# Optimization experiments

Measured on AMD Instinct MI355X. Metric: run time of the kernel, lower is better.

The kernel has to match this reference:

```python
import jax, jax.numpy as jnp
import numpy as np

N_NODES = 100000
NEG_SLOPE = 0.2  # PyG GATConv default LeakyReLU slope


def gat_conv(x, src, dst, W, a_src, a_dst, bias, n):
    # x: [N, Fin] -> h: [N, Fout]; heads=1, concat=True (PyG defaults), add_self_loops=False
    h = x @ W
    alpha_s = h @ a_src  # [N]
    alpha_d = h @ a_dst  # [N]
    e = jax.nn.leaky_relu(alpha_s[src] + alpha_d[dst], NEG_SLOPE)  # [E]
    # segment-softmax over edges grouped by destination node
    m = jax.ops.segment_max(e, dst, num_segments=n)  # [N], -inf for isolated nodes (never gathered)
    ex = jnp.exp(e - m[dst])
    denom = jax.ops.segment_sum(ex, dst, num_segments=n)
    alpha = ex / denom[dst]  # [E]
    out = jax.ops.segment_sum(alpha[:, None] * h[src], dst, num_segments=n)
    return out + bias


def setup_inputs() -> dict:
    key = jax.random.key(0)
    ks = jax.random.split(key, 12)
    n, e, fin, hid, ncls = N_NODES, 6400000, 128, 8, 16
    x = jax.random.normal(ks[0], (n, fin), dtype=jnp.float32)
    edge_index = jax.random.randint(ks[1], (2, e), 0, n, dtype=jnp.int32)
    s1 = 1.0 / np.sqrt(fin)
    s2 = 1.0 / np.sqrt(hid)
    return {
        "x": x,
        "edge_index": edge_index,
        "W1": jax.random.normal(ks[2], (fin, hid), dtype=jnp.float32) * s1,
        "a1_src": jax.random.normal(ks[3], (hid,), dtype=jnp.float32) * s2,
        "a1_dst": jax.random.normal(ks[4], (hid,), dtype=jnp.float32) * s2,
        "b1": jnp.zeros((hid,), dtype=jnp.float32),
        "W2": jax.random.normal(ks[5], (hid, ncls), dtype=jnp.float32) * s2,
        "a2_src": jax.random.normal(ks[6], (ncls,), dtype=jnp.float32) * 0.25,
        "a2_dst": jax.random.normal(ks[7], (ncls,), dtype=jnp.float32) * 0.25,
        "b2": jnp.zeros((ncls,), dtype=jnp.float32),
    }


def reference(x, edge_index, W1, a1_src, a1_dst, b1, W2, a2_src, a2_dst, b2):
    src, dst = edge_index[0], edge_index[1]
    n = x.shape[0]
    h = jax.nn.relu(gat_conv(x, src, dst, W1, a1_src, a1_dst, b1, n))
    # F.dropout(training=False) in inference -> identity
    out = gat_conv(h, src, dst, W2, a2_src, a2_dst, b2, n)
    return jax.nn.log_softmax(out, axis=1)
```

## Files before the change

### kernel.cpp

```cpp
#include <hip/hip_runtime.h>
#include <hip/hip_fp16.h>
#include <math.h>
#include <stdint.h>

#define NEG 0.2f
#define CSHIFT 7
#define BUCKN (1 << CSHIFT)
#define MAXNB 1024
#define CHUNK 4096
#define FBUF 9216


__global__ __launch_bounds__(256) void k1_node(const float* __restrict__ x,
    const float* __restrict__ W1, const float* __restrict__ a1s, const float* __restrict__ a1d,
    float4* __restrict__ h1pk, float* __restrict__ ad1, int n)
{
    __shared__ float wt[8 * 128];
    __shared__ float av[16];
    for (int i = threadIdx.x; i < 1024; i += 256) {
        int r = i >> 3, k = i & 7;
        wt[k * 128 + r] = W1[i];
    }
    if (threadIdx.x < 8)        av[threadIdx.x] = a1s[threadIdx.x];
    else if (threadIdx.x < 16)  av[threadIdx.x] = a1d[threadIdx.x - 8];
    __syncthreads();

    int lane = threadIdx.x & 31;
    int node = blockIdx.x * 8 + (threadIdx.x >> 5);
    if (node >= n) return;

    float4 xv = ((const float4*)(x + (size_t)node * 128))[lane];
    float p[8];
#pragma unroll
    for (int k = 0; k < 8; ++k) {
        float4 wv = ((const float4*)(wt + k * 128))[lane];
        p[k] = xv.x * wv.x + xv.y * wv.y + xv.z * wv.z + xv.w * wv.w;
    }
#pragma unroll
    for (int off = 16; off; off >>= 1)
#pragma unroll
        for (int k = 0; k < 8; ++k) p[k] += __shfl_down(p[k], off, 32);

    if (lane == 0) {
        float s = 0.f, d = 0.f;
        union { float4 f; __half2 h[4]; } u;
#pragma unroll
        for (int k = 0; k < 8; ++k) {
            s += p[k] * av[k];
            d += p[k] * av[8 + k];
        }
#pragma unroll
        for (int q = 0; q < 4; ++q) u.h[q] = __floats2half2_rn(p[2 * q], p[2 * q + 1]);
        h1pk[2 * (size_t)node]     = u.f;
        h1pk[2 * (size_t)node + 1] = make_float4(s, 0.f, 0.f, 0.f);
        ad1[node] = d;
    }
}


__global__ __launch_bounds__(256) void p1a(const int* __restrict__ dst, int* __restrict__ gmat,
                                           int E, int NB)
{
    __shared__ int h[MAXNB];
    for (int i = threadIdx.x; i < NB; i += 256) h[i] = 0;
    __syncthreads();
    int base = blockIdx.x * CHUNK;
    int end = base + CHUNK; if (end > E) end = E;
    for (int i = base + threadIdx.x; i < end; i += 256)
        atomicAdd(&h[dst[i] >> CSHIFT], 1);
    __syncthreads();
    int* row = gmat + (size_t)blockIdx.x * NB;
    for (int i = threadIdx.x; i < NB; i += 256) row[i] = h[i];
}

__global__ __launch_bounds__(256) void pcol(const int* __restrict__ gmat, int* __restrict__ pbaseRel,
    int* __restrict__ total, int NBLK, int NB)
{
    __shared__ int wsum[4];
    int b = blockIdx.x;
    int tid = threadIdx.x;
    int chunk = (NBLK + 255) >> 8;
    int k0 = tid * chunk;
    int s = 0;
    for (int j = 0; j < chunk; ++j) {
        int k = k0 + j;
        if (k < NBLK) s += gmat[(size_t)k * NB + b];
    }
    int lane = tid & 63, w = tid >> 6;
    int sc = s;
#pragma unroll
    for (int off = 1; off < 64; off <<= 1) {
        int t = __shfl_up(sc, off, 64);
        if (lane >= off) sc += t;
    }
    if (lane == 63) wsum[w] = sc;
    __syncthreads();
    if (tid == 0) { int a = 0; for (int i = 0; i < 4; ++i) { int t = wsum[i]; wsum[i] = a; a += t; } }
    __syncthreads();
    int run = sc - s + wsum[w];
    for (int j = 0; j < chunk; ++j) {
        int k = k0 + j;
        if (k < NBLK) {
            int gv = gmat[(size_t)k * NB + b];
            pbaseRel[(size_t)k * NB + b] = run;
            run += gv;
        }
    }
    if (tid == 255) total[b] = run;
}

__global__ __launch_bounds__(512) void ptot(const int* __restrict__ total, int* __restrict__ cptr,
                                            int* __restrict__ row_ptr, int NB, int n, int E)
{
    __shared__ int wsum[8];
    int tid = threadIdx.x;
    int chunk = (NB + 511) >> 9;
    int k0 = tid * chunk;
    int s = 0;
    for (int j = 0; j < chunk; ++j) {
        int k = k0 + j;
        if (k < NB) s += total[k];
    }
    int lane = tid & 63, w = tid >> 6;
    int sc = s;
#pragma unroll
    for (int off = 1; off < 64; off <<= 1) {
        int t = __shfl_up(sc, off, 64);
        if (lane >= off) sc += t;
    }
    if (lane == 63) wsum[w] = sc;
    __syncthreads();
    if (tid == 0) { int a = 0; for (int i = 0; i < 8; ++i) { int t = wsum[i]; wsum[i] = a; a += t; } }
    __syncthreads();
    int run = sc - s + wsum[w];
    for (int j = 0; j < chunk; ++j) {
        int k = k0 + j;
        if (k < NB) { cptr[k] = run; run += total[k]; }
    }
    if (tid == 0) { cptr[NB] = E; row_ptr[n] = E; }
}

__global__ __launch_bounds__(256) void p1bW(const int* __restrict__ src, const int* __restrict__ dst,
    const int* __restrict__ gmat, const int* __restrict__ cptr, const int* __restrict__ pbaseRel,
    unsigned* __restrict__ stage, int E, int NB)
{
    __shared__ int lbase[MAXNB], bbase[MAXNB], ccur[MAXNB];
    __shared__ unsigned bufp[CHUNK];
    __shared__ unsigned short bufb[CHUNK];
    __shared__ int wsum[4];
    int tid = threadIdx.x;
    const int* grow = gmat + (size_t)blockIdx.x * NB;
    const int* prow = pbaseRel + (size_t)blockIdx.x * NB;

    int base = blockIdx.x * CHUNK;
    int end = base + CHUNK; if (end > E) end = E;
    int cnt = end - base;

    int chunkb = (NB + 255) >> 8;
    int b0 = tid * chunkb;
    int s = 0;
    for (int j = 0; j < chunkb; ++j) {
        int b = b0 + j;
        if (b < NB) s += grow[b];
    }
    int lane = tid & 63, w = tid >> 6;
    int sc = s;
#pragma unroll
    for (int off = 1; off < 64; off <<= 1) {
        int t = __shfl_up(sc, off, 64);
        if (lane >= off) sc += t;
    }
    if (lane == 63) wsum[w] = sc;
    __syncthreads();
    if (tid == 0) { int a = 0; for (int i = 0; i < 4; ++i) { int t = wsum[i]; wsum[i] = a; a += t; } }
    __syncthreads();
    int run = sc - s + wsum[w];
    for (int j = 0; j < chunkb; ++j) {
        int b = b0 + j;
        if (b < NB) {
            lbase[b] = run;
            run += grow[b];
            bbase[b] = cptr[b] + prow[b];
            ccur[b] = 0;
        }
    }
    __syncthreads();

    for (int i = base + tid; i < end; i += 256) {
        int d = dst[i];
        int b = d >> CSHIFT;
        int off = atomicAdd(&ccur[b], 1);
        int pos = lbase[b] + off;
        bufp[pos] = ((unsigned)(d & (BUCKN - 1)) << 17) | (unsigned)src[i];
        bufb[pos] = (unsigned short)b;
    }
    __syncthreads();

    for (int i = tid; i < cnt; i += 256) {
        int b = bufb[i];
        stage[bbase[b] + (i - lbase[b])] = bufp[i];
    }
}

__global__ __launch_bounds__(512) void p2(const unsigned* __restrict__ stage,
    const int* __restrict__ cptr, int* __restrict__ colsrc, int* __restrict__ row_ptr, int n)
{
    int b = blockIdx.x;
    int nbase = b << CSHIFT;
    int NN = n - nbase; if (NN > BUCKN) NN = BUCKN;
    __shared__ int h[BUCKN], bps[BUCKN], cc[BUCKN];
    __shared__ int wsum[2];
    __shared__ int buf[FBUF];
    int tid = threadIdx.x;
    if (tid < BUCKN) { h[tid] = 0; cc[tid] = 0; }
    __syncthreads();
    int s0 = cptr[b], s1 = cptr[b + 1];
    int span = s1 - s0;
    for (int i = s0 + tid; i < s1; i += 512)
        atomicAdd(&h[stage[i] >> 17], 1);
    __syncthreads();
    if (tid < BUCKN) {
        int v = h[tid];
        int lane = tid & 63, w = tid >> 6;
        int sc = v;
#pragma unroll
        for (int off = 1; off < 64; off <<= 1) {
            int t = __shfl_up(sc, off, 64);
            if (lane >= off) sc += t;
        }
        if (lane == 63) wsum[w] = sc;
        __syncthreads();
        if (tid == 0) { int a = 0; for (int i = 0; i < 2; ++i) { int t = wsum[i]; wsum[i] = a; a += t; } }
        __syncthreads();
        int excl = sc - v + wsum[w];
        bps[tid] = excl;
        if (tid < NN) row_ptr[nbase + tid] = s0 + excl;
    } else {
        __syncthreads();
        __syncthreads();
    }
    __syncthreads();

    if (span <= FBUF) {
        for (int i = s0 + tid; i < s1; i += 512) {
            unsigned p = stage[i];
            int f = p >> 17;
            int off = atomicAdd(&cc[f], 1);
            buf[bps[f] + off] = (int)(p & 0x1FFFFu);
        }
        __syncthreads();
        for (int i = tid; i < span; i += 512)
            colsrc[s0 + i] = buf[i];
    } else {
        for (int i = s0 + tid; i < s1; i += 512) {
            unsigned p = stage[i];
            int f = p >> 17;
            int off = atomicAdd(&cc[f], 1);
            colsrc[s0 + bps[f] + off] = (int)(p & 0x1FFFFu);
        }
    }
}


__global__ __launch_bounds__(256) void k_gather8f(const int* __restrict__ row_ptr,
    const int* __restrict__ colsrc, const float4* __restrict__ featpk, const float* __restrict__ ad,
    const float* __restrict__ b1, const float* __restrict__ W2,
    const float* __restrict__ a2s, const float* __restrict__ a2d,
    float4* __restrict__ outpk, float* __restrict__ ad2, int n)
{
    __shared__ float w2as[8], w2ad[8], b1v[8];
    if (threadIdx.x < 8) {
        float s = 0.f, d = 0.f;
#pragma unroll
        for (int c = 0; c < 16; ++c) {
            float wv = W2[threadIdx.x * 16 + c];
            s += wv * a2s[c];
            d += wv * a2d[c];
        }
        w2as[threadIdx.x] = s;
        w2ad[threadIdx.x] = d;
        b1v[threadIdx.x] = b1[threadIdx.x];
    }
    __syncthreads();

    int wid  = (blockIdx.x * 256 + threadIdx.x) >> 6;
    int lane = threadIdx.x & 63;
    int l16  = lane & 15;
    int node = wid * 4 + (lane >> 4);
    bool active = node < n;

    int start = 0, end = 0;
    float adn = 0.f;
    if (active) { start = row_ptr[node]; end = row_ptr[node + 1]; adn = ad[node]; }

    float wsum = 0.f, acc[8];
#pragma unroll
    for (int k = 0; k < 8; ++k) acc[k] = 0.f;

    for (int i = start + l16; i < end; i += 16) {
        int s = colsrc[i];
        union { float4 fv; __half2 h[4]; } u;
        u.fv = featpk[2 * (size_t)s];
        float4 meta = featpk[2 * (size_t)s + 1];
        float t = meta.x + adn;
        float w = __expf(t > 0.f ? t : NEG * t);
        wsum += w;
#pragma unroll
        for (int q = 0; q < 4; ++q) {
            float2 hv = __half22float2(u.h[q]);
            acc[2 * q + 0] += w * hv.x;
            acc[2 * q + 1] += w * hv.y;
        }
    }
#pragma unroll
    for (int off = 8; off; off >>= 1) {
        wsum += __shfl_xor(wsum, off, 64);
#pragma unroll
        for (int k = 0; k < 8; ++k) acc[k] += __shfl_xor(acc[k], off, 64);
    }
    if (!active || l16 != 0) return;

    float inv = wsum > 0.f ? 1.f / wsum : 0.f;
    float h[8], s2 = 0.f, d2 = 0.f;
    union { float4 f; __half2 hh[4]; } u;
#pragma unroll
    for (int k = 0; k < 8; ++k) {
        float v = acc[k] * inv + b1v[k];
        h[k] = v > 0.f ? v : 0.f;
        s2 += h[k] * w2as[k];
        d2 += h[k] * w2ad[k];
    }
#pragma unroll
    for (int q = 0; q < 4; ++q) u.hh[q] = __floats2half2_rn(h[2 * q], h[2 * q + 1]);
    outpk[2 * (size_t)node]     = u.f;
    outpk[2 * (size_t)node + 1] = make_float4(s2, 0.f, 0.f, 0.f);
    ad2[node] = d2;
}

__global__ __launch_bounds__(256) void k_gather16(const int* __restrict__ row_ptr,
    const int* __restrict__ colsrc, const float4* __restrict__ featpk, const float* __restrict__ ad,
    const float* __restrict__ W2, const float* __restrict__ bias, float* __restrict__ outp, int n)
{
    __shared__ float w2s[128], bv[16];
    if (threadIdx.x < 128) w2s[threadIdx.x] = W2[threadIdx.x];
    else if (threadIdx.x < 144) bv[threadIdx.x - 128] = bias[threadIdx.x - 128];
    __syncthreads();

    int wid  = (blockIdx.x * 256 + threadIdx.x) >> 6;
    int lane = threadIdx.x & 63;
    int l16  = lane & 15;
    int node = wid * 4 + (lane >> 4);
    bool active = node < n;

    int start = 0, end = 0;
    float adn = 0.f;
    if (active) { start = row_ptr[node]; end = row_ptr[node + 1]; adn = ad[node]; }

    float wsum = 0.f, acc[8];
#pragma unroll
    for (int k = 0; k < 8; ++k) acc[k] = 0.f;

    for (int i = start + l16; i < end; i += 16) {
        int s = colsrc[i];
        union { float4 fv; __half2 h[4]; } u;
        u.fv = featpk[2 * (size_t)s];
        float4 meta = featpk[2 * (size_t)s + 1];
        float t = meta.x + adn;
        float w = __expf(t > 0.f ? t : NEG * t);
        wsum += w;
#pragma unroll
        for (int q = 0; q < 4; ++q) {
            float2 hv = __half22float2(u.h[q]);
            acc[2 * q + 0] += w * hv.x;
            acc[2 * q + 1] += w * hv.y;
        }
    }
#pragma unroll
    for (int off = 8; off; off >>= 1) {
        wsum += __shfl_xor(wsum, off, 64);
#pragma unroll
        for (int k = 0; k < 8; ++k) acc[k] += __shfl_xor(acc[k], off, 64);
    }
    if (!active) return;

    float inv = wsum > 0.f ? 1.f / wsum : 0.f;
    float o = bv[l16];
#pragma unroll
    for (int k = 0; k < 8; ++k) o += (acc[k] * inv) * w2s[k * 16 + l16];
    float m = o;
#pragma unroll
    for (int off = 8; off; off >>= 1) m = fmaxf(m, __shfl_xor(m, off, 64));
    float se = __expf(o - m);
#pragma unroll
    for (int off = 8; off; off >>= 1) se += __shfl_xor(se, off, 64);
    float l = m + __logf(se);
    outp[(size_t)node * 16 + l16] = o - l;
}


__global__ __launch_bounds__(256) void k1_nodeF(const float* __restrict__ x,
    const float* __restrict__ W1, const float* __restrict__ a1s, const float* __restrict__ a1d,
    float* __restrict__ h1, float* __restrict__ as1, float* __restrict__ ad1, int n)
{
    __shared__ float wt[8 * 128];
    __shared__ float av[16];
    for (int i = threadIdx.x; i < 1024; i += 256) {
        int r = i >> 3, k = i & 7;
        wt[k * 128 + r] = W1[i];
    }
    if (threadIdx.x < 8)        av[threadIdx.x] = a1s[threadIdx.x];
    else if (threadIdx.x < 16)  av[threadIdx.x] = a1d[threadIdx.x - 8];
    __syncthreads();

    int lane = threadIdx.x & 31;
    int node = blockIdx.x * 8 + (threadIdx.x >> 5);
    if (node >= n) return;

    float4 xv = ((const float4*)(x + (size_t)node * 128))[lane];
    float p[8];
#pragma unroll
    for (int k = 0; k < 8; ++k) {
        float4 wv = ((const float4*)(wt + k * 128))[lane];
        p[k] = xv.x * wv.x + xv.y * wv.y + xv.z * wv.z + xv.w * wv.w;
    }
#pragma unroll
    for (int off = 16; off; off >>= 1)
#pragma unroll
        for (int k = 0; k < 8; ++k) p[k] += __shfl_down(p[k], off, 32);

    if (lane == 0) {
        float s = 0.f, d = 0.f;
#pragma unroll
        for (int k = 0; k < 8; ++k) {
            h1[(size_t)node * 8 + k] = p[k];
            s += p[k] * av[k];
            d += p[k] * av[8 + k];
        }
        as1[node] = s;
        ad1[node] = d;
    }
}

template <int F>
__global__ __launch_bounds__(256) void k_edge(const int* __restrict__ src, const int* __restrict__ dst,
    const float* __restrict__ as, const float* __restrict__ ad, const float* __restrict__ feat,
    float* __restrict__ denom, float* __restrict__ acc, int E)
{
    int e = blockIdx.x * 256 + threadIdx.x;
    if (e >= E) return;
    int s = src[e], d = dst[e];
    float t = as[s] + ad[d];
    float w = __expf(t > 0.f ? t : NEG * t);
    atomicAdd(denom + d, w);
    const float* fs = feat + (size_t)s * F;
    float* ac = acc + (size_t)d * F;
#pragma unroll
    for (int k = 0; k < F; ++k) atomicAdd(ac + k, w * fs[k]);
}

__global__ __launch_bounds__(256) void k3_node(const float* __restrict__ denom1,
    const float* __restrict__ acc1, const float* __restrict__ b1,
    const float* __restrict__ W2, const float* __restrict__ a2s, const float* __restrict__ a2d,
    float* __restrict__ g, float* __restrict__ as2, float* __restrict__ ad2, int n)
{
    __shared__ float w2[128];
    __shared__ float aa[32];
    __shared__ float bb[8];
    if (threadIdx.x < 128) w2[threadIdx.x] = W2[threadIdx.x];
    if (threadIdx.x >= 128 && threadIdx.x < 144) aa[threadIdx.x - 128] = a2s[threadIdx.x - 128];
    if (threadIdx.x >= 144 && threadIdx.x < 160) aa[16 + threadIdx.x - 144] = a2d[threadIdx.x - 144];
    if (threadIdx.x >= 160 && threadIdx.x < 168) bb[threadIdx.x - 160] = b1[threadIdx.x - 160];
    __syncthreads();

    int node = blockIdx.x * 256 + threadIdx.x;
    if (node >= n) return;
    float dn = denom1[node];
    float inv = dn > 0.f ? 1.f / dn : 0.f;
    float h[8];
#pragma unroll
    for (int k = 0; k < 8; ++k) {
        float v = acc1[(size_t)node * 8 + k] * inv + bb[k];
        h[k] = v > 0.f ? v : 0.f;
    }
    float s = 0.f, dd = 0.f;
#pragma unroll
    for (int c = 0; c < 16; ++c) {
        float gv = 0.f;
#pragma unroll
        for (int k = 0; k < 8; ++k) gv += h[k] * w2[k * 16 + c];
        g[(size_t)node * 16 + c] = gv;
        s += gv * aa[c];
        dd += gv * aa[16 + c];
    }
    as2[node] = s;
    ad2[node] = dd;
}

__global__ __launch_bounds__(256) void k5_final(const float* __restrict__ denom2,
    const float* __restrict__ acc2, const float* __restrict__ b2, float* __restrict__ out, int n)
{
    __shared__ float bb[16];
    if (threadIdx.x < 16) bb[threadIdx.x] = b2[threadIdx.x];
    __syncthreads();

    int node = blockIdx.x * 256 + threadIdx.x;
    if (node >= n) return;
    float dn = denom2[node];
    float inv = dn > 0.f ? 1.f / dn : 0.f;
    float o[16];
    float m = -1e30f;
#pragma unroll
    for (int c = 0; c < 16; ++c) {
        o[c] = acc2[(size_t)node * 16 + c] * inv + bb[c];
        m = fmaxf(m, o[c]);
    }
    float se = 0.f;
#pragma unroll
    for (int c = 0; c < 16; ++c) {
        o[c] -= m;
        se += __expf(o[c]);
    }
    float l = __logf(se);
#pragma unroll
    for (int c = 0; c < 16; ++c) out[(size_t)node * 16 + c] = o[c] - l;
}


static inline char* align256(char* p) {
    return (char*)(((uintptr_t)p + 255) & ~(uintptr_t)255);
}

extern "C" void kernel_launch(void* const* d_in, const int* in_sizes, int n_in,
                              void* d_out, int out_size, void* d_ws, size_t ws_size,
                              hipStream_t stream)
{
    const float* x    = (const float*)d_in[0];
    const int*   eidx = (const int*)d_in[1];
    const float* W1   = (const float*)d_in[2];
    const float* a1s  = (const float*)d_in[3];
    const float* a1d  = (const float*)d_in[4];
    const float* b1   = (const float*)d_in[5];
    const float* W2   = (const float*)d_in[6];
    const float* a2s  = (const float*)d_in[7];
    const float* a2d  = (const float*)d_in[8];
    const float* b2   = (const float*)d_in[9];
    float* out = (float*)d_out;

    const int n = in_sizes[0] / 128;
    const int E = in_sizes[1] / 2;
    const int* src = eidx;
    const int* dst = eidx + E;
    const int NB = (n + BUCKN - 1) >> CSHIFT;
    const int NBLK = (E + CHUNK - 1) / CHUNK;

    {
        char* p = (char*)d_ws;
        char* p0 = p;
        unsigned* stage = (unsigned*)p;  p = align256(p + (size_t)E * 4);
        int* colsrc  = (int*)p;          p = align256(p + (size_t)E * 4);
        int* total   = (int*)p;          p = align256(p + (size_t)NB * 4);
        int* cptr    = (int*)p;          p = align256(p + (size_t)(NB + 1) * 4);
        int* row_ptr = (int*)p;          p = align256(p + (size_t)(n + 1) * 4);
        float4* h1pk  = (float4*)p;      p = align256(p + (size_t)n * 32);
        float4* h1ppk = (float4*)p;      p = align256(p + (size_t)n * 32);
        float* ad1   = (float*)p;        p = align256(p + (size_t)n * 4);
        float* ad2   = (float*)p;        p = align256(p + (size_t)n * 4);
        size_t needed = (size_t)(p - p0);

        int* gmat     = colsrc;
        int* pbaseRel = (int*)align256((char*)(colsrc + (size_t)NBLK * NB));

        bool alias_ok = ((size_t)2 * NBLK * NB + 64) <= (size_t)E;

        if (n <= 131072 && NB <= MAXNB && alias_ok && ws_size >= needed) {
            k1_node<<<(n + 7) / 8, 256, 0, stream>>>(x, W1, a1s, a1d, h1pk, ad1, n);

            p1a<<<NBLK, 256, 0, stream>>>(dst, gmat, E, NB);
            pcol<<<NB, 256, 0, stream>>>(gmat, pbaseRel, total, NBLK, NB);
            ptot<<<1, 512, 0, stream>>>(total, cptr, row_ptr, NB, n, E);
            p1bW<<<NBLK, 256, 0, stream>>>(src, dst, gmat, cptr, pbaseRel, stage, E, NB);
            p2<<<NB, 512, 0, stream>>>(stage, cptr, colsrc, row_ptr, n);

            const int gblocks = ((size_t)n * 16 + 255) / 256;
            k_gather8f<<<gblocks, 256, 0, stream>>>(row_ptr, colsrc, h1pk, ad1,
                                                    b1, W2, a2s, a2d, h1ppk, ad2, n);
            k_gather16<<<gblocks, 256, 0, stream>>>(row_ptr, colsrc, h1ppk, ad2, W2, b2, out, n);
            return;
        }
    }

    {
        float* ws     = (float*)d_ws;
        float* denom1 = ws;
        float* acc1   = ws + (size_t)n;
        float* denom2 = ws + (size_t)9 * n;
        float* acc2   = ws + (size_t)10 * n;
        float* h1     = ws + (size_t)26 * n;
        float* as1    = ws + (size_t)34 * n;
        float* ad1    = ws + (size_t)35 * n;
        float* g      = ws + (size_t)36 * n;
        float* as2    = ws + (size_t)52 * n;
        float* ad2    = ws + (size_t)53 * n;

        hipMemsetAsync(ws, 0, (size_t)26 * n * sizeof(float), stream);
        k1_nodeF<<<(n + 7) / 8, 256, 0, stream>>>(x, W1, a1s, a1d, h1, as1, ad1, n);
        k_edge<8><<<(E + 255) / 256, 256, 0, stream>>>(src, dst, as1, ad1, h1, denom1, acc1, E);
        k3_node<<<(n + 255) / 256, 256, 0, stream>>>(denom1, acc1, b1, W2, a2s, a2d, g, as2, ad2, n);
        k_edge<16><<<(E + 255) / 256, 256, 0, stream>>>(src, dst, as2, ad2, g, denom2, acc2, E);
        k5_final<<<(n + 255) / 256, 256, 0, stream>>>(denom2, acc2, b2, out, n);
    }
}
```

Measured before the change: 215.3 us.

## Use coarser 512-node dst buckets and split CSR fill into four sub-blocks

Raises the dst bucket size from 128 to 512 nodes, which cuts the number of buckets the partition passes (p1a/pcol/p1bW) have to histogram and scatter. The second-stage sort kernel now runs four blocks per bucket. Each block rebuilds the full 512-entry histogram and prefix scan, but only places edges whose local node falls in its own 128-node quarter, staging them in shared memory. In exchange, every sub-block rereads the whole bucket's staged edges, so stage traffic in p2 is four times higher, while the partition passes get fewer bucket counters.

```diff
diff --git a/kernel.cpp b/kernel.cpp
--- a/kernel.cpp
+++ b/kernel.cpp
@@ -4,9 +4,9 @@
 #include <stdint.h>
 
 #define NEG 0.2f
-#define CSHIFT 7
+#define CSHIFT 9
 #define BUCKN (1 << CSHIFT)
-#define MAXNB 1024
+#define MAXNB 256
 #define CHUNK 4096
 #define FBUF 9216
 
@@ -202,61 +202,74 @@
     }
 }
 
-__global__ __launch_bounds__(512) void p2(const unsigned* __restrict__ stage,
+__global__ __launch_bounds__(512) void p2s(const unsigned* __restrict__ stage,
     const int* __restrict__ cptr, int* __restrict__ colsrc, int* __restrict__ row_ptr, int n)
 {
-    int b = blockIdx.x;
-    int nbase = b << CSHIFT;
-    int NN = n - nbase; if (NN > BUCKN) NN = BUCKN;
-    __shared__ int h[BUCKN], bps[BUCKN], cc[BUCKN];
-    __shared__ int wsum[2];
+    int b = blockIdx.x >> 2;
+    int j = blockIdx.x & 3;
+    int nbase = (b << CSHIFT) + j * 128;
+    __shared__ int h[BUCKN], cc[128];
+    __shared__ int wsum[8];
     __shared__ int buf[FBUF];
     int tid = threadIdx.x;
-    if (tid < BUCKN) { h[tid] = 0; cc[tid] = 0; }
+    h[tid] = 0;
+    if (tid < 128) cc[tid] = 0;
     __syncthreads();
     int s0 = cptr[b], s1 = cptr[b + 1];
     int span = s1 - s0;
+
     for (int i = s0 + tid; i < s1; i += 512)
         atomicAdd(&h[stage[i] >> 17], 1);
     __syncthreads();
-    if (tid < BUCKN) {
-        int v = h[tid];
-        int lane = tid & 63, w = tid >> 6;
-        int sc = v;
-#pragma unroll
-        for (int off = 1; off < 64; off <<= 1) {
-            int t = __shfl_up(sc, off, 64);
-            if (lane >= off) sc += t;
-        }
-        if (lane == 63) wsum[w] = sc;
-        __syncthreads();
-        if (tid == 0) { int a = 0; for (int i = 0; i < 2; ++i) { int t = wsum[i]; wsum[i] = a; a += t; } }
-        __syncthreads();
-        int excl = sc - v + wsum[w];
-        bps[tid] = excl;
-        if (tid < NN) row_ptr[nbase + tid] = s0 + excl;
-    } else {
-        __syncthreads();
-        __syncthreads();
-    }
-    __syncthreads();
-
-    if (span <= FBUF) {
+
+    int v = h[tid];
+    int lane = tid & 63, w = tid >> 6;
+    int sc = v;
+#pragma unroll
+    for (int off = 1; off < 64; off <<= 1) {
+        int t = __shfl_up(sc, off, 64);
+        if (lane >= off) sc += t;
+    }
+    if (lane == 63) wsum[w] = sc;
+    __syncthreads();
+    if (tid == 0) { int a = 0; for (int i = 0; i < 8; ++i) { int t = wsum[i]; wsum[i] = a; a += t; } }
+    __syncthreads();
+    int excl = sc - v + wsum[w];
+    h[tid] = excl;
+    __syncthreads();
+
+    int q0 = j * 128;
+    int substart = h[q0];
+    int subend = (j == 3) ? span : h[q0 + 128];
+    int subspan = subend - substart;
+
+    if (tid < 128) {
+        int node = nbase + tid;
+        if (node < n) row_ptr[node] = s0 + h[q0 + tid];
+    }
+    __syncthreads();
+
+    if (subspan <= FBUF) {
         for (int i = s0 + tid; i < s1; i += 512) {
             unsigned p = stage[i];
             int f = p >> 17;
-            int off = atomicAdd(&cc[f], 1);
-            buf[bps[f] + off] = (int)(p & 0x1FFFFu);
+            if ((f >> 7) == j) {
+                int off = atomicAdd(&cc[f & 127], 1);
+                buf[h[f] - substart + off] = (int)(p & 0x1FFFFu);
+            }
         }
         __syncthreads();
-        for (int i = tid; i < span; i += 512)
-            colsrc[s0 + i] = buf[i];
+        int gbase = s0 + substart;
+        for (int i = tid; i < subspan; i += 512)
+            colsrc[gbase + i] = buf[i];
     } else {
         for (int i = s0 + tid; i < s1; i += 512) {
             unsigned p = stage[i];
             int f = p >> 17;
-            int off = atomicAdd(&cc[f], 1);
-            colsrc[s0 + bps[f] + off] = (int)(p & 0x1FFFFu);
+            if ((f >> 7) == j) {
+                int off = atomicAdd(&cc[f & 127], 1);
+                colsrc[s0 + h[f] + off] = (int)(p & 0x1FFFFu);
+            }
         }
     }
 }
@@ -579,7 +592,7 @@
             pcol<<<NB, 256, 0, stream>>>(gmat, pbaseRel, total, NBLK, NB);
             ptot<<<1, 512, 0, stream>>>(total, cptr, row_ptr, NB, n, E);
             p1bW<<<NBLK, 256, 0, stream>>>(src, dst, gmat, cptr, pbaseRel, stage, E, NB);
-            p2<<<NB, 512, 0, stream>>>(stage, cptr, colsrc, row_ptr, n);
+            p2s<<<NB * 4, 512, 0, stream>>>(stage, cptr, colsrc, row_ptr, n);
 
             const int gblocks = ((size_t)n * 16 + 255) / 256;
             k_gather8f<<<gblocks, 256, 0, stream>>>(row_ptr, colsrc, h1pk, ad1,
```

Result: no change. 216.3 us (+0.5%).
